# Kernel tuning notes

Hardware: AMD Instinct MI355X
Metric: run time of the kernel (lower is better)

## Reference

```python
import jax, jax.numpy as jnp
import numpy as np
import math

B, N, M, Lx = 8, 32, 16, 32
D, TE_DIM, IN_DIM, TT = 64, 16, 17, 63   # hid_dim, te_dim, 1+te_dim, hid_dim-1
H, DH, NL = 4, 16, 2
TAU, DELTA = 60.0, 300.0                 # tau, 5 minutes in seconds
P = B * N * M


def _ln(x, g, b):
    mu = x.mean(-1, keepdims=True)
    v = ((x - mu) ** 2).mean(-1, keepdims=True)
    return (x - mu) / jnp.sqrt(v + 1e-5) * g + b


def _time_bias():
    idx = jnp.arange(M)
    dist = jnp.abs(idx[:, None] - idx[None, :]).astype(jnp.float32) * DELTA
    return jnp.log(jnp.exp(-dist / TAU) + 1e-12)


def _pos_enc():
    pos = jnp.arange(M, dtype=jnp.float32)[:, None]
    div = jnp.exp(jnp.arange(0, D, 2, dtype=jnp.float32) * (-math.log(10000.0) / D))
    pe = jnp.zeros((M, D))
    pe = pe.at[:, 0::2].set(jnp.sin(pos * div))
    pe = pe.at[:, 1::2].set(jnp.cos(pos * div))
    return pe


def _heads(t):   # (b, m, D) -> (b, H, m, DH)
    b, m, _ = t.shape
    return t.reshape(b, m, H, DH).transpose(0, 2, 1, 3)


def _merge(t):   # (b, H, m, DH) -> (b, m, D)
    b, _, m, _ = t.shape
    return t.transpose(0, 2, 1, 3).reshape(b, m, D)


def _patch_gattn(x, pm, qw, qb, kw, kb, vw, vb, ow, ob, tbias):
    q, k, v = _heads(x @ qw.T + qb), _heads(x @ kw.T + kb), _heads(x @ vw.T + vb)
    a = jnp.einsum('bhqd,bhkd->bhqk', q, k) / math.sqrt(DH) + tbias[None, None]
    a = jnp.where((pm == 0.0)[:, None, None, :], -1e9, a)
    out = _merge(jnp.einsum('bhqk,bhkd->bhqd', jax.nn.softmax(a, -1), v))
    return (out @ ow.T + ob) * pm[..., None]


def _mha(q_in, kv_in, in_w, in_b, ow, ob, kpm=None):
    wq, wk, wv = in_w[:D], in_w[D:2 * D], in_w[2 * D:]
    bq, bk, bv = in_b[:D], in_b[D:2 * D], in_b[2 * D:]
    q = _heads(q_in @ wq.T + bq)
    k = _heads(kv_in @ wk.T + bk)
    v = _heads(kv_in @ wv.T + bv)
    a = jnp.einsum('bhqd,bhkd->bhqk', q, k) / math.sqrt(DH)
    if kpm is not None:
        a = jnp.where(kpm[:, None, None, :], -1e9, a)
    out = _merge(jnp.einsum('bhqk,bhkd->bhqd', jax.nn.softmax(a, -1), v))
    return out @ ow.T + ob


def _forward(x, mask, ttcn_w1, ttcn_b1, ttcn_w2, ttcn_b2, ttcn_w3, ttcn_b3, t_bias,
             ga_qw, ga_qb, ga_kw, ga_kb, ga_vw, ga_vb, ga_ow, ga_ob,
             tf_in_w, tf_in_b, tf_out_w, tf_out_b, tf_ln1_g, tf_ln1_b, tf_ln2_g, tf_ln2_b,
             tf_fw1, tf_fb1, tf_fw2, tf_fb2,
             q_embed, cls_in_w, cls_in_b, cls_out_w, cls_out_b, logit_w, logit_b):
    m = mask.astype(x.dtype)                          # (P, Lx, 1)
    # --- TTCN: per-sample dynamic filter generation + masked seq-softmax agg ---
    h = jax.nn.relu(x @ ttcn_w1.T + ttcn_b1)
    h = jax.nn.relu(h @ ttcn_w2.T + ttcn_b2)
    filt = h @ ttcn_w3.T + ttcn_b3                    # (P, Lx, IN_DIM*TT)
    filt = filt * m + (1.0 - m) * (-1e8)
    fs = jax.nn.softmax(filt, axis=1).reshape(P, Lx, TT, IN_DIM)
    h_t = jax.nn.relu(jnp.einsum('pli,plti->pt', x, fs) + t_bias)   # (P, TT)
    mask_patch = (m.sum(axis=1) > 0).astype(x.dtype)  # (P, 1)
    xp = jnp.concatenate([h_t, mask_patch], -1).reshape(B, N, M, D)
    pm = mask_patch.reshape(B, N, M)
    tbias = _time_bias()
    pe = _pos_enc()
    xc = xp
    for l in range(NL):
        if l > 0:
            x_last = xc
        xb = xc.reshape(B * N, M, D)
        pmb = pm.reshape(B * N, M)
        xb = xb + _patch_gattn(xb, pmb, ga_qw[l], ga_qb[l], ga_kw[l], ga_kb[l],
                               ga_vw[l], ga_vb[l], ga_ow[l], ga_ob[l], tbias)
        xb = xb + pe[None]
        # post-norm TransformerEncoderLayer (tf_layer = 1, no attn mask, eval mode)
        attn = _mha(xb, xb, tf_in_w[l], tf_in_b[l], tf_out_w[l], tf_out_b[l])
        xb = _ln(xb + attn, tf_ln1_g[l], tf_ln1_b[l])
        ff = jax.nn.relu(xb @ tf_fw1[l].T + tf_fb1[l]) @ tf_fw2[l].T + tf_fb2[l]
        xb = _ln(xb + ff, tf_ln2_g[l], tf_ln2_b[l])
        xc = xb.reshape(B, N, M, D)
        if l > 0:
            xc = x_last + xc
    x_seq = xc.mean(axis=1)                            # (B, M, D)
    kpm = ~((pm > 0).any(axis=1))                      # (B, M), True = padded
    qs = jnp.broadcast_to(q_embed[None], (B, 5, D))
    z = _mha(qs, x_seq, cls_in_w, cls_in_b, cls_out_w, cls_out_b, kpm=kpm)
    return (z @ logit_w.T + logit_b)[..., 0]           # (B, 5)


def setup_inputs() -> dict:
    key = jax.random.key(0)
    ks = iter(jax.random.split(key, 64))
    def rn(shape, s=0.1):
        return jax.random.normal(next(ks), shape, jnp.float32) * s
    inp = {
        'x': jax.random.normal(next(ks), (P, Lx, IN_DIM), jnp.float32),
        'mask': jax.random.randint(next(ks), (P, Lx, 1), 0, 2, jnp.int32),
        'ttcn_w1': rn((TT, IN_DIM)), 'ttcn_b1': jnp.zeros((TT,)),
        'ttcn_w2': rn((TT, TT)), 'ttcn_b2': jnp.zeros((TT,)),
        'ttcn_w3': rn((IN_DIM * TT, TT)), 'ttcn_b3': jnp.zeros((IN_DIM * TT,)),
        't_bias': rn((1, TT)),
        'ga_qw': rn((NL, D, D)), 'ga_qb': jnp.zeros((NL, D)),
        'ga_kw': rn((NL, D, D)), 'ga_kb': jnp.zeros((NL, D)),
        'ga_vw': rn((NL, D, D)), 'ga_vb': jnp.zeros((NL, D)),
        'ga_ow': rn((NL, D, D)), 'ga_ob': jnp.zeros((NL, D)),
        'tf_in_w': rn((NL, 3 * D, D)), 'tf_in_b': jnp.zeros((NL, 3 * D)),
        'tf_out_w': rn((NL, D, D)), 'tf_out_b': jnp.zeros((NL, D)),
        'tf_ln1_g': jnp.ones((NL, D)), 'tf_ln1_b': jnp.zeros((NL, D)),
        'tf_ln2_g': jnp.ones((NL, D)), 'tf_ln2_b': jnp.zeros((NL, D)),
        'tf_fw1': rn((NL, 2048, D)), 'tf_fb1': jnp.zeros((NL, 2048)),
        'tf_fw2': rn((NL, D, 2048)), 'tf_fb2': jnp.zeros((NL, D)),
        'q_embed': rn((5, D), 1.0),
        'cls_in_w': rn((3 * D, D)), 'cls_in_b': jnp.zeros((3 * D,)),
        'cls_out_w': rn((D, D)), 'cls_out_b': jnp.zeros((D,)),
        'logit_w': rn((1, D)), 'logit_b': jnp.zeros((1,)),
    }
    return inp


def reference(x, mask, ttcn_w1, ttcn_b1, ttcn_w2, ttcn_b2, ttcn_w3, ttcn_b3, t_bias,
              ga_qw, ga_qb, ga_kw, ga_kb, ga_vw, ga_vb, ga_ow, ga_ob,
              tf_in_w, tf_in_b, tf_out_w, tf_out_b, tf_ln1_g, tf_ln1_b, tf_ln2_g, tf_ln2_b,
              tf_fw1, tf_fb1, tf_fw2, tf_fb2,
              q_embed, cls_in_w, cls_in_b, cls_out_w, cls_out_b, logit_w, logit_b):
    return _forward(x, mask, ttcn_w1, ttcn_b1, ttcn_w2, ttcn_b2, ttcn_w3, ttcn_b3, t_bias,
                    ga_qw, ga_qb, ga_kw, ga_kb, ga_vw, ga_vb, ga_ow, ga_ob,
                    tf_in_w, tf_in_b, tf_out_w, tf_out_b, tf_ln1_g, tf_ln1_b, tf_ln2_g, tf_ln2_b,
                    tf_fw1, tf_fb1, tf_fw2, tf_fb2,
                    q_embed, cls_in_w, cls_in_b, cls_out_w, cls_out_b, logit_w, logit_b)
```

## Files before the change

kernel.cpp:

```cpp
#include <hip/hip_runtime.h>
#include <hip/hip_bf16.h>
#include <math.h>

#define B_  8
#define N_  32
#define M_  16
#define LX  32
#define D_  64
#define IN_DIM_ 17
#define TT_ 63
#define H_  4
#define DH_ 16
#define P_TOT 4096
#define BN_ 256
#define FF_ 2048

#define FRAG_TOT 83200
#define OFF_INW  2048
#define OFF_OUTW 3584
#define OFF_FW1  4096
#define OFF_FW2  20480

typedef unsigned short ushort_t;
typedef __attribute__((ext_vector_type(8))) short short8;
typedef __attribute__((ext_vector_type(4))) float floatx4;

#define MFMA16(a,b,c) __builtin_amdgcn_mfma_f32_16x16x32_bf16((a),(b),(c),0,0,0)

__device__ __forceinline__ float fast_exp2(float x){
#if __has_builtin(__builtin_amdgcn_exp2f)
  return __builtin_amdgcn_exp2f(x);
#else
  return __expf(x * 0.6931471805599453f);
#endif
}
__device__ __forceinline__ float fast_rcp(float x){
#if __has_builtin(__builtin_amdgcn_rcpf)
  return __builtin_amdgcn_rcpf(x);
#else
  return 1.0f / x;
#endif
}

__device__ __forceinline__ ushort_t f2bf(float f){
  unsigned u = __float_as_uint(f);
  u += 0x7FFFu + ((u >> 16) & 1u);
  return (ushort_t)(u >> 16);
}
__device__ __forceinline__ float bf2f(ushort_t h){ return __uint_as_float(((unsigned)h) << 16); }

__device__ __forceinline__ uint4 pack8(const ushort_t* h){
  uint4 u;
  u.x = (unsigned)h[0] | ((unsigned)h[1] << 16);
  u.y = (unsigned)h[2] | ((unsigned)h[3] << 16);
  u.z = (unsigned)h[4] | ((unsigned)h[5] << 16);
  u.w = (unsigned)h[6] | ((unsigned)h[7] << 16);
  return u;
}

__device__ __forceinline__ void split8(const float* r, short8& hi, short8& lo){
  #pragma unroll
  for (int j = 0; j < 8; ++j){
    float v = r[j];
    ushort_t h = f2bf(v);
    ushort_t l2 = f2bf(v - bf2f(h));
    hi[j] = (short)h; lo[j] = (short)l2;
  }
}
__device__ __forceinline__ uint4 cvt8(const float* r){
  ushort_t hh[8];
  #pragma unroll
  for (int j = 0; j < 8; ++j) hh[j] = f2bf(r[j]);
  return pack8(hh);
}
__device__ __forceinline__ short8 cvt8s(const float* r){
  union { uint4 u4; short8 s8; } cv;
  cv.u4 = cvt8(r);
  return cv.s8;
}

__device__ __forceinline__ floatx4 mm3(short8 ah, short8 al, short8 bh, short8 bl, floatx4 c){
  c = MFMA16(ah, bh, c); c = MFMA16(ah, bl, c); c = MFMA16(al, bh, c); return c;
}

__device__ __forceinline__ float dot64(const float* __restrict__ a, const float* __restrict__ w){
  const float4* a4 = (const float4*)a;
  const float4* w4 = (const float4*)w;
  float acc = 0.f;
  #pragma unroll
  for (int k = 0; k < 16; ++k){ float4 x = a4[k], y = w4[k];
    acc += x.x*y.x + x.y*y.y + x.z*y.z + x.w*y.w; }
  return acc;
}
__device__ __forceinline__ float dot16(const float* __restrict__ a, const float* __restrict__ b){
  const float4* a4 = (const float4*)a; const float4* b4 = (const float4*)b;
  float acc = 0.f;
  #pragma unroll
  for (int k = 0; k < 4; ++k){ float4 x = a4[k], y = b4[k];
    acc += x.x*y.x + x.y*y.y + x.z*y.z + x.w*y.w; }
  return acc;
}

__device__ __forceinline__ void packA68(const float* buf, short8* fA, int tid){
  if (tid < 128){
    int ln = tid & 63, ks = tid >> 6;
    const float* r = buf + (ln & 15)*68 + ks*32 + ((ln >> 4) & 3)*8;
    short8 hi, lo; split8(r, hi, lo);
    fA[tid] = hi; fA[128 + tid] = lo;
  }
}

__global__ __launch_bounds__(256) void prep_kernel(
    const float* __restrict__ w1, const float* __restrict__ w2, const float* __restrict__ w3,
    const float* __restrict__ gqw, const float* __restrict__ gkw,
    const float* __restrict__ gvw, const float* __restrict__ gow,
    const float* __restrict__ inw, const float* __restrict__ outw,
    const float* __restrict__ fw1, const float* __restrict__ fw2,
    uint4* __restrict__ fr)
{
  int s = blockIdx.x*256 + threadIdx.x;
  if (s >= FRAG_TOT) return;
  const float* src; int Nr, Kr, KS, rel; int w3seg = 0, noLo = 0;
  if (s < 256)      { src = w1; Nr=63;  Kr=17; KS=1; rel = s; noLo = 1; }
  else if (s < 768) { src = w2; Nr=63;  Kr=63; KS=2; rel = s-256; noLo = 1; }
  else if (s < 9472){ src = w3; Nr=1071;Kr=63; KS=2; rel = s-768; w3seg = 1; noLo = 1; }
  else {
    int t = s - 9472, l = t / 36864, r2 = t - l*36864;
    if (r2 < 512)        { src = gqw + l*4096;   Nr=64;  Kr=64;   KS=2;  rel = r2; }
    else if (r2 < 1024)  { src = gkw + l*4096;   Nr=64;  Kr=64;   KS=2;  rel = r2-512; }
    else if (r2 < 1536)  { src = gvw + l*4096;   Nr=64;  Kr=64;   KS=2;  rel = r2-1024; }
    else if (r2 < 2048)  { src = gow + l*4096;   Nr=64;  Kr=64;   KS=2;  rel = r2-1536; }
    else if (r2 < 3584)  { src = inw + l*12288;  Nr=192; Kr=64;   KS=2;  rel = r2-2048; }
    else if (r2 < 4096)  { src = outw + l*4096;  Nr=64;  Kr=64;   KS=2;  rel = r2-3584; }
    else if (r2 < 20480) { src = fw1 + l*131072; Nr=2048;Kr=64;   KS=2;  rel = r2-4096; noLo = 1; }
    else                 { src = fw2 + l*131072; Nr=64;  Kr=2048; KS=64; rel = r2-20480; noLo = 1; }
  }
  int lane = rel & 63, tmp = rel >> 6;
  int ks = tmp % KS, nt = tmp / KS;
  int kb = ks*32 + ((lane >> 4) & 3)*8;
  int n, validn;
  if (w3seg){
    int i = nt >> 2, tq = nt & 3;
    int t = tq*16 + (lane & 15);
    n = t*17 + i;
    validn = (t < 63);
  } else {
    n = nt*16 + (lane & 15);
    validn = (n < Nr);
  }
  float v[8];
  #pragma unroll
  for (int j = 0; j < 8; ++j){
    v[j] = (validn && (kb + j) < Kr) ? src[n*Kr + kb + j] : 0.f;
    if (w3seg){
      if ((kb + j) == 63) v[j] = 1.0f;
      v[j] *= 1.4426950408889634f;
    }
  }
  ushort_t hh[8];
  #pragma unroll
  for (int j = 0; j < 8; ++j) hh[j] = f2bf(v[j]);
  fr[s] = pack8(hh);
  if (!noLo){
    ushort_t ll[8];
    #pragma unroll
    for (int j = 0; j < 8; ++j) ll[j] = f2bf(v[j] - bf2f(hh[j]));
    fr[FRAG_TOT + s] = pack8(ll);
  }
}

__global__ __launch_bounds__(256) void ttcn_kernel(
    const float* __restrict__ x, const int* __restrict__ mask,
    const float* __restrict__ b1, const float* __restrict__ b2,
    const float* __restrict__ tb,
    const short8* __restrict__ w1bhi,
    const short8* __restrict__ w2bhi,
    const short8* __restrict__ w3bhi,
    float* __restrict__ xp, float* __restrict__ pm)
{
  __shared__ __align__(16) char pool[16512];
  float*    xs    = (float*)(pool + 0);
  float*    xst   = (float*)(pool + 2560);
  float*    msv   = (float*)(pool + 5008);
  float*    xsumv = (float*)(pool + 5136);
  short8*   xfhi  = (short8*)(pool + 5216);
  ushort_t* h1t   = (ushort_t*)(pool + 7264);
  ushort_t* h2t   = (ushort_t*)(pool + 11872);

  const int p = blockIdx.x, tid = threadIdx.x;
  const int lane = tid & 63, wvi = tid >> 6;
  const int nidx = lane & 15, quad = lane >> 4;

  for (int idx = tid; idx < LX*IN_DIM_; idx += 256){
    int l = (idx * 3856) >> 16;
    int i = idx - l*17;
    xs[l*20 + i] = x[p*(LX*IN_DIM_) + idx];
  }
  if (tid < LX) msv[tid] = (float)mask[p*LX + tid];
  __syncthreads();

  if (tid < 128){
    int mt = tid >> 6;
    int l = mt*16 + nidx;
    float r[8];
    #pragma unroll
    for (int j = 0; j < 8; ++j){
      int k = quad*8 + j;
      r[j] = (k < IN_DIM_) ? xs[l*20 + k] : 0.f;
    }
    ((uint4*)xfhi)[tid] = cvt8(r);
  } else {
    if (tid < 128 + IN_DIM_){
      int i = tid - 128;
      float s = 0.f;
      #pragma unroll
      for (int l = 0; l < LX; ++l) s += xs[l*20 + i];
      xsumv[i] = s;
    }
    for (int idx = tid - 128; idx < 544; idx += 128){
      int i = idx >> 5, l = idx & 31;
      xst[i*36 + l] = xs[l*20 + i];
    }
  }
  __syncthreads();

  {
    short8 axh0 = xfhi[lane], axh1 = xfhi[64 + lane];
    short8 bh = w1bhi[wvi*64 + lane];
    floatx4 a0 = {0.f,0.f,0.f,0.f}, a1 = {0.f,0.f,0.f,0.f};
    a0 = MFMA16(axh0, bh, a0);
    a1 = MFMA16(axh1, bh, a1);
    int t = wvi*16 + nidx;
    float bb = (t < TT_) ? b1[t] : 0.f;
    #pragma unroll
    for (int r = 0; r < 4; ++r){
      h1t[(quad*4+r)*72 + t]      = f2bf(fmaxf(a0[r] + bb, 0.f));
      h1t[(16+quad*4+r)*72 + t]   = f2bf(fmaxf(a1[r] + bb, 0.f));
    }
  }
  __syncthreads();

  {
    short8 ah[2][2];
    #pragma unroll
    for (int mt = 0; mt < 2; ++mt)
      #pragma unroll
      for (int ks = 0; ks < 2; ++ks){
        int l = mt*16 + nidx;
        ah[mt][ks] = *(const short8*)((const char*)h1t + (l*72 + ks*32 + quad*8)*2);
      }
    short8 bh0 = w2bhi[(wvi*2+0)*64 + lane];
    short8 bh1 = w2bhi[(wvi*2+1)*64 + lane];
    floatx4 a0 = {0.f,0.f,0.f,0.f}, a1 = {0.f,0.f,0.f,0.f};
    a0 = MFMA16(ah[0][0], bh0, a0); a0 = MFMA16(ah[0][1], bh1, a0);
    a1 = MFMA16(ah[1][0], bh0, a1); a1 = MFMA16(ah[1][1], bh1, a1);
    int t = wvi*16 + nidx;
    float bb = (t < TT_) ? b2[t] : 0.f;
    #pragma unroll
    for (int r = 0; r < 4; ++r){
      h2t[(quad*4+r)*72 + t]      = f2bf(fmaxf(a0[r] + bb, 0.f));
      h2t[(16+quad*4+r)*72 + t]   = f2bf(fmaxf(a1[r] + bb, 0.f));
    }
  }
  __syncthreads();

  {
    short8 ah[2][2];
    #pragma unroll
    for (int mt = 0; mt < 2; ++mt)
      #pragma unroll
      for (int ks = 0; ks < 2; ++ks){
        int l = mt*16 + nidx;
        ah[mt][ks] = *(const short8*)((const char*)h2t + (l*72 + ks*32 + quad*8)*2);
      }
    if (quad == 3){
      ah[0][1][7] = (short)((msv[nidx]      == 0.f) ? f2bf(-1e8f) : (ushort_t)0);
      ah[1][1][7] = (short)((msv[16 + nidx] == 0.f) ? f2bf(-1e8f) : (ushort_t)0);
    }
    const int t_out = wvi*16 + nidx;
    const int rA = quad*4;
    float acc_t = 0.f;
    short8 nbh0 = w3bhi[(wvi*2+0)*64 + lane];
    short8 nbh1 = w3bhi[(wvi*2+1)*64 + lane];
    for (int it = 0; it < 17; ++it){
      short8 bh0 = nbh0, bh1 = nbh1;
      if (it < 16){
        int nt = wvi + it*4 + 4;
        nbh0 = w3bhi[(nt*2+0)*64 + lane];
        nbh1 = w3bhi[(nt*2+1)*64 + lane];
      }
      floatx4 a0 = {0.f,0.f,0.f,0.f}, a1 = {0.f,0.f,0.f,0.f};
      a0 = MFMA16(ah[0][0], bh0, a0); a0 = MFMA16(ah[0][1], bh1, a0);
      a1 = MFMA16(ah[1][0], bh0, a1); a1 = MFMA16(ah[1][1], bh1, a1);

      const float4 xA = *(const float4*)(xst + it*36 + rA);
      const float4 xB = *(const float4*)(xst + it*36 + rA + 16);
      float den0 = 0.f, den1 = 0.f, num0 = 0.f, num1 = 0.f;
      float e;
      e = fast_exp2(a0[0]); den0 += e; num0 = fmaf(e, xA.x, num0);
      e = fast_exp2(a0[1]); den0 += e; num0 = fmaf(e, xA.y, num0);
      e = fast_exp2(a0[2]); den0 += e; num0 = fmaf(e, xA.z, num0);
      e = fast_exp2(a0[3]); den0 += e; num0 = fmaf(e, xA.w, num0);
      e = fast_exp2(a1[0]); den1 += e; num1 = fmaf(e, xB.x, num1);
      e = fast_exp2(a1[1]); den1 += e; num1 = fmaf(e, xB.y, num1);
      e = fast_exp2(a1[2]); den1 += e; num1 = fmaf(e, xB.z, num1);
      e = fast_exp2(a1[3]); den1 += e; num1 = fmaf(e, xB.w, num1);
      float den = den0 + den1, num = num0 + num1;
      den += __shfl_xor(den, 16, 64); den += __shfl_xor(den, 32, 64);
      num += __shfl_xor(num, 16, 64); num += __shfl_xor(num, 32, 64);
      float res = (den > 0.f) ? num * fast_rcp(den) : xsumv[it] * (1.f/32.f);
      acc_t += res;
    }
    if (quad == 0 && t_out < TT_)
      xp[p*D_ + t_out] = fmaxf(acc_t + tb[t_out], 0.f);
  }
  if (tid == 63){
    float s = 0.f;
    #pragma unroll
    for (int l = 0; l < LX; ++l) s += msv[l];
    float mp = (s > 0.f) ? 1.f : 0.f;
    xp[p*D_ + TT_] = mp;
    pm[p] = mp;
  }
}

__global__ __launch_bounds__(256) void layer12_kernel(
    const float* __restrict__ xin, const float* __restrict__ pm,
    const short8* __restrict__ frS,
    const float* __restrict__ gqb, const float* __restrict__ gkb,
    const float* __restrict__ gvb, const float* __restrict__ gob,
    const float* __restrict__ inb, const float* __restrict__ outb,
    const float* __restrict__ ln1g, const float* __restrict__ ln1b,
    const float* __restrict__ fb1, const float* __restrict__ fb2,
    const float* __restrict__ ln2g, const float* __restrict__ ln2b,
    float* __restrict__ xout)
{
  __shared__ __align__(16) float xb[16*68];
  __shared__ __align__(16) float xb2[16*68];
  __shared__ __align__(16) float q_[16*68];
  __shared__ __align__(16) float k_[16*68];
  __shared__ __align__(16) float v_[16*68];
  __shared__ __align__(16) float ao[16*68];
  __shared__ __align__(16) float ss[1024];
  __shared__ __align__(16) short8 fragA[256];
  __shared__ __align__(16) float hbuf[4*16*36];
  __shared__ __align__(16) float part[4*16*68];
  __shared__ __align__(16) float pe_t[1024];
  __shared__ float tbt[16];
  __shared__ float pmv[16], mur[16], rvr[16];

  const int bn = blockIdx.x, tid = threadIdx.x;
  const int lane = tid & 63, wvi = tid >> 6;
  const int nidx = lane & 15, quad = lane >> 4;
  const float* xin_p = xin + bn*1024;

  for (int o = tid; o < 1024; o += 256) xb[(o>>6)*68 + (o&63)] = xin_p[o];
  if (tid < 16) pmv[tid] = pm[bn*16 + tid];
  for (int o = tid; o < 1024; o += 256){
    int tok = o >> 6, d = o & 63;
    float div = __expf((float)(d & ~1) * (-0.14391156831212793f));
    float arg = (float)tok * div;
    pe_t[o] = (d & 1) ? cosf(arg) : sinf(arg);
  }
  if (tid >= 32 && tid < 48) tbt[tid-32] = logf(expf(-5.0f*(float)(tid-32)) + 1e-12f);
  __syncthreads();

  for (int l = 0; l < 2; ++l){
    const int lbase = 9472 + l*36864;
    const float* gqbL = gqb + l*64;  const float* gkbL = gkb + l*64;
    const float* gvbL = gvb + l*64;  const float* gobL = gob + l*64;
    const float* inbL = inb + l*192; const float* outbL = outb + l*64;
    const float* ln1gL = ln1g + l*64; const float* ln1bL = ln1b + l*64;
    const float* fb1L = fb1 + l*2048; const float* fb2L = fb2 + l*64;
    const float* ln2gL = ln2g + l*64; const float* ln2bL = ln2b + l*64;

    float xres[4];
    #pragma unroll
    for (int kk2 = 0; kk2 < 4; ++kk2){
      int o = tid + kk2*256;
      xres[kk2] = xb[(o>>6)*68 + (o&63)];
    }

    short8 gb[3][4], ob4[4], mb[3][4];
    #pragma unroll
    for (int mat = 0; mat < 3; ++mat){
      int base = lbase + mat*512;
      gb[mat][0] = frS[base + (wvi*2+0)*64 + lane];
      gb[mat][1] = frS[FRAG_TOT + base + (wvi*2+0)*64 + lane];
      gb[mat][2] = frS[base + (wvi*2+1)*64 + lane];
      gb[mat][3] = frS[FRAG_TOT + base + (wvi*2+1)*64 + lane];
    }
    {
      int base = lbase + 1536;
      ob4[0] = frS[base + (wvi*2+0)*64 + lane];
      ob4[1] = frS[FRAG_TOT + base + (wvi*2+0)*64 + lane];
      ob4[2] = frS[base + (wvi*2+1)*64 + lane];
      ob4[3] = frS[FRAG_TOT + base + (wvi*2+1)*64 + lane];
    }
    #pragma unroll
    for (int sel = 0; sel < 3; ++sel){
      int base = lbase + OFF_INW + (sel*4 + wvi)*128;
      mb[sel][0] = frS[base + lane];
      mb[sel][1] = frS[FRAG_TOT + base + lane];
      mb[sel][2] = frS[base + 64 + lane];
      mb[sel][3] = frS[FRAG_TOT + base + 64 + lane];
    }

    packA68(xb, fragA, tid);
    __syncthreads();
    {
      short8 axh0 = fragA[lane], axh1 = fragA[64+lane];
      short8 axl0 = fragA[128+lane], axl1 = fragA[192+lane];
      #pragma unroll
      for (int mat = 0; mat < 3; ++mat){
        floatx4 c = {0.f,0.f,0.f,0.f};
        c = mm3(axh0, axl0, gb[mat][0], gb[mat][1], c);
        c = mm3(axh1, axl1, gb[mat][2], gb[mat][3], c);
        int d = wvi*16 + nidx;
        float bb = (mat == 0 ? gqbL : mat == 1 ? gkbL : gvbL)[d];
        float* dst = (mat == 0 ? q_ : mat == 1 ? k_ : v_);
        #pragma unroll
        for (int r = 0; r < 4; ++r) dst[(quad*4+r)*68 + d] = c[r] + bb;
      }
    }
    __syncthreads();
    {
      int row = tid >> 2;
      int h = row >> 4, qm = row & 15;
      int km0 = (tid & 3) * 4;
      float s4[4];
      #pragma unroll
      for (int j = 0; j < 4; ++j){
        int km = km0 + j;
        float acc = dot16(q_ + qm*68 + h*16, k_ + km*68 + h*16);
        int dd = qm - km; if (dd < 0) dd = -dd;
        acc = acc * 0.25f + tbt[dd];
        if (pmv[km] == 0.f) acc = -1e9f;
        s4[j] = acc;
      }
      float mx = fmaxf(fmaxf(s4[0], s4[1]), fmaxf(s4[2], s4[3]));
      mx = fmaxf(mx, __shfl_xor(mx, 1, 64));
      mx = fmaxf(mx, __shfl_xor(mx, 2, 64));
      float e4[4], se = 0.f;
      #pragma unroll
      for (int j = 0; j < 4; ++j){ e4[j] = __expf(s4[j]-mx); se += e4[j]; }
      se += __shfl_xor(se, 1, 64);
      se += __shfl_xor(se, 2, 64);
      float inv = fast_rcp(se);
      #pragma unroll
      for (int j = 0; j < 4; ++j) ss[row*16 + km0 + j] = e4[j]*inv;
    }
    __syncthreads();
    for (int o = tid; o < 1024; o += 256){
      int m = o >> 6, d = o & 63, h = d >> 4;
      float acc = 0.f;
      #pragma unroll
      for (int km = 0; km < 16; ++km) acc += ss[h*256 + m*16 + km] * v_[km*68 + d];
      ao[m*68 + d] = acc;
    }
    __syncthreads();
    packA68(ao, fragA, tid);
    __syncthreads();
    {
      short8 axh0 = fragA[lane], axh1 = fragA[64+lane];
      short8 axl0 = fragA[128+lane], axl1 = fragA[192+lane];
      floatx4 c = {0.f,0.f,0.f,0.f};
      c = mm3(axh0, axl0, ob4[0], ob4[1], c);
      c = mm3(axh1, axl1, ob4[2], ob4[3], c);
      int d = wvi*16 + nidx;
      float bb = gobL[d];
      #pragma unroll
      for (int r = 0; r < 4; ++r){
        int tok = quad*4 + r;
        xb[tok*68 + d] += (c[r] + bb) * pmv[tok] + pe_t[tok*64 + d];
      }
    }
    __syncthreads();

    short8 mob[4], f1c[4], f2c[4];
    {
      int base = lbase + OFF_OUTW;
      mob[0] = frS[base + (wvi*2+0)*64 + lane];
      mob[1] = frS[FRAG_TOT + base + (wvi*2+0)*64 + lane];
      mob[2] = frS[base + (wvi*2+1)*64 + lane];
      mob[3] = frS[FRAG_TOT + base + (wvi*2+1)*64 + lane];
    }
    {
      int f1base = lbase + OFF_FW1, f2base = lbase + OFF_FW2;
      #pragma unroll
      for (int t2 = 0; t2 < 2; ++t2){
        int sb = f1base + ((wvi*32+t2)*2)*64 + lane;
        f1c[t2*2+0] = frS[sb];
        f1c[t2*2+1] = frS[sb + 64];
      }
      #pragma unroll
      for (int ntd = 0; ntd < 4; ++ntd)
        f2c[ntd] = frS[f2base + (ntd*64 + wvi*16)*64 + lane];
    }

    packA68(xb, fragA, tid);
    __syncthreads();
    {
      short8 axh0 = fragA[lane], axh1 = fragA[64+lane];
      short8 axl0 = fragA[128+lane], axl1 = fragA[192+lane];
      #pragma unroll
      for (int sel = 0; sel < 3; ++sel){
        floatx4 c = {0.f,0.f,0.f,0.f};
        c = mm3(axh0, axl0, mb[sel][0], mb[sel][1], c);
        c = mm3(axh1, axl1, mb[sel][2], mb[sel][3], c);
        int d = wvi*16 + nidx;
        float bb = inbL[(sel*4 + wvi)*16 + nidx];
        float* dst = (sel == 0 ? q_ : sel == 1 ? k_ : v_);
        #pragma unroll
        for (int r = 0; r < 4; ++r) dst[(quad*4+r)*68 + d] = c[r] + bb;
      }
    }
    __syncthreads();
    {
      int row = tid >> 2;
      int h = row >> 4, qm = row & 15;
      int km0 = (tid & 3) * 4;
      float s4[4];
      #pragma unroll
      for (int j = 0; j < 4; ++j)
        s4[j] = 0.25f * dot16(q_ + qm*68 + h*16, k_ + (km0+j)*68 + h*16);
      float mx = fmaxf(fmaxf(s4[0], s4[1]), fmaxf(s4[2], s4[3]));
      mx = fmaxf(mx, __shfl_xor(mx, 1, 64));
      mx = fmaxf(mx, __shfl_xor(mx, 2, 64));
      float e4[4], se = 0.f;
      #pragma unroll
      for (int j = 0; j < 4; ++j){ e4[j] = __expf(s4[j]-mx); se += e4[j]; }
      se += __shfl_xor(se, 1, 64);
      se += __shfl_xor(se, 2, 64);
      float inv = fast_rcp(se);
      #pragma unroll
      for (int j = 0; j < 4; ++j) ss[row*16 + km0 + j] = e4[j]*inv;
    }
    __syncthreads();
    for (int o = tid; o < 1024; o += 256){
      int m = o >> 6, d = o & 63, h = d >> 4;
      float acc = 0.f;
      #pragma unroll
      for (int km = 0; km < 16; ++km) acc += ss[h*256 + m*16 + km] * v_[km*68 + d];
      ao[m*68 + d] = acc;
    }
    __syncthreads();
    packA68(ao, fragA, tid);
    __syncthreads();
    {
      short8 axh0 = fragA[lane], axh1 = fragA[64+lane];
      short8 axl0 = fragA[128+lane], axl1 = fragA[192+lane];
      floatx4 c = {0.f,0.f,0.f,0.f};
      c = mm3(axh0, axl0, mob[0], mob[1], c);
      c = mm3(axh1, axl1, mob[2], mob[3], c);
      int d = wvi*16 + nidx;
      float bb = outbL[d];
      #pragma unroll
      for (int r = 0; r < 4; ++r) xb[(quad*4+r)*68 + d] += c[r] + bb;
    }
    __syncthreads();

    if (tid < 64){
      int row = tid >> 2, seg = tid & 3;
      const float* rp = xb + row*68 + seg*16;
      float s = 0.f;
      #pragma unroll
      for (int j = 0; j < 16; ++j) s += rp[j];
      s += __shfl_xor(s, 1, 64); s += __shfl_xor(s, 2, 64);
      float mu = s * (1.f/64.f);
      float v = 0.f;
      #pragma unroll
      for (int j = 0; j < 16; ++j){ float t = rp[j]-mu; v += t*t; }
      v += __shfl_xor(v, 1, 64); v += __shfl_xor(v, 2, 64);
      if (seg == 0){ mur[row] = mu; rvr[row] = rsqrtf(v*(1.f/64.f) + 1e-5f); }
    }
    __syncthreads();
    for (int o = tid; o < 1024; o += 256){
      int m = o >> 6, d = o & 63;
      xb2[m*68 + d] = (xb[m*68 + d] - mur[m]) * rvr[m] * ln1gL[d] + ln1bL[d];
    }
    __syncthreads();
    packA68(xb2, fragA, tid);
    __syncthreads();

    {
      const int w = wvi;
      const int f1base = lbase + OFF_FW1, f2base = lbase + OFF_FW2;
      short8 axh0 = fragA[lane], axh1 = fragA[64 + lane];
      floatx4 y0 = {0.f,0.f,0.f,0.f}, y1 = y0, y2 = y0, y3 = y0;
      float* hw = hbuf + w*576;

      short8 f1n[4], f2n[4];
      for (int it = 0; it < 16; ++it){
        int ntA = w*32 + it*2;
        floatx4 hA = {0.f,0.f,0.f,0.f}, hB = hA;
        hA = MFMA16(axh0, f1c[0], hA); hA = MFMA16(axh1, f1c[1], hA);
        hB = MFMA16(axh0, f1c[2], hB); hB = MFMA16(axh1, f1c[3], hB);
        float bbA = fb1L[ntA*16 + nidx], bbB = fb1L[ntA*16 + 16 + nidx];
        #pragma unroll
        for (int r = 0; r < 4; ++r){
          hw[(quad*4+r)*36 + nidx]      = fmaxf(hA[r] + bbA, 0.f);
          hw[(quad*4+r)*36 + 16 + nidx] = fmaxf(hB[r] + bbB, 0.f);
        }
        if (it < 15){
          int ntN = ntA + 2, kstN = w*16 + it + 1;
          #pragma unroll
          for (int t2 = 0; t2 < 2; ++t2){
            int sb = f1base + ((ntN+t2)*2)*64 + lane;
            f1n[t2*2+0] = frS[sb];
            f1n[t2*2+1] = frS[sb + 64];
          }
          #pragma unroll
          for (int ntd = 0; ntd < 4; ++ntd)
            f2n[ntd] = frS[f2base + (ntd*64 + kstN)*64 + lane];
        }
        short8 ah = cvt8s(hw + (lane & 15)*36 + quad*8);
        y0 = MFMA16(ah, f2c[0], y0);
        y1 = MFMA16(ah, f2c[1], y1);
        y2 = MFMA16(ah, f2c[2], y2);
        y3 = MFMA16(ah, f2c[3], y3);
        #pragma unroll
        for (int j = 0; j < 4; ++j){ f1c[j] = f1n[j]; f2c[j] = f2n[j]; }
      }
      #pragma unroll
      for (int r = 0; r < 4; ++r){
        int row = (quad*4 + r)*68;
        part[w*1088 + row + nidx]      = y0[r];
        part[w*1088 + row + 16 + nidx] = y1[r];
        part[w*1088 + row + 32 + nidx] = y2[r];
        part[w*1088 + row + 48 + nidx] = y3[r];
      }
    }
    __syncthreads();
    for (int o = tid; o < 1024; o += 256){
      int tok = o >> 6, d = o & 63;
      float s = xb2[tok*68 + d] + fb2L[d];
      #pragma unroll
      for (int ww = 0; ww < 4; ++ww) s += part[ww*1088 + tok*68 + d];
      xb[tok*68 + d] = s;
    }
    __syncthreads();
    if (tid < 64){
      int row = tid >> 2, seg = tid & 3;
      const float* rp = xb + row*68 + seg*16;
      float s = 0.f;
      #pragma unroll
      for (int j = 0; j < 16; ++j) s += rp[j];
      s += __shfl_xor(s, 1, 64); s += __shfl_xor(s, 2, 64);
      float mu = s * (1.f/64.f);
      float v = 0.f;
      #pragma unroll
      for (int j = 0; j < 16; ++j){ float t = rp[j]-mu; v += t*t; }
      v += __shfl_xor(v, 1, 64); v += __shfl_xor(v, 2, 64);
      if (seg == 0){ mur[row] = mu; rvr[row] = rsqrtf(v*(1.f/64.f) + 1e-5f); }
    }
    __syncthreads();
    #pragma unroll
    for (int kk2 = 0; kk2 < 4; ++kk2){
      int o = tid + kk2*256;
      int tok = o >> 6, d = o & 63;
      float vv = (xb[tok*68 + d] - mur[tok]) * rvr[tok] * ln2gL[d] + ln2bL[d];
      if (l == 0) xb[tok*68 + d] = vv;
      else        xout[bn*1024 + o] = vv + xres[kk2];
    }
    __syncthreads();
  }
}

__global__ __launch_bounds__(256) void final_kernel(
    const float* __restrict__ xc, const float* __restrict__ pm,
    const float* __restrict__ q_embed,
    const float* __restrict__ cin_w, const float* __restrict__ cin_b,
    const float* __restrict__ cout_w, const float* __restrict__ cout_b,
    const float* __restrict__ logit_w, const float* __restrict__ logit_b,
    float* __restrict__ out)
{
  const int b = blockIdx.x;
  const int tid = threadIdx.x;
  __shared__ __align__(16) float xs[M_ * D_];
  __shared__ float kpmv[M_];
  __shared__ __align__(16) float qv[5 * D_], kv[M_ * D_], vv[M_ * D_];
  __shared__ float sv[H_ * 5 * M_];
  __shared__ __align__(16) float ao[5 * D_], zv[5 * D_];

  for (int o = tid; o < M_ * D_; o += 256) {
    int m = o >> 6, d = o & 63;
    float acc = 0.f;
    #pragma unroll
    for (int n = 0; n < N_; ++n) acc += xc[(((b * N_ + n) * M_ + m) * D_) + d];
    xs[o] = acc * (1.f / 32.f);
  }
  if (tid < M_) {
    float any = 0.f;
    #pragma unroll
    for (int n = 0; n < N_; ++n) any += (pm[(b * N_ + n) * M_ + tid] > 0.f) ? 1.f : 0.f;
    kpmv[tid] = (any > 0.f) ? 0.f : 1.f;
  }
  __syncthreads();

  for (int o = tid; o < 5 * D_; o += 256) {
    int qi = o >> 6, d = o & 63;
    qv[o] = cin_b[d] + dot64(q_embed + qi * D_, cin_w + d * D_);
  }
  for (int o = tid; o < 2 * M_ * D_; o += 256) {
    int sel = o >> 10, r = o & 1023, m = r >> 6, d = r & 63;
    float acc = cin_b[D_ + sel * D_ + d] + dot64(xs + m * D_, cin_w + (D_ + sel * D_ + d) * D_);
    ((sel == 0) ? kv : vv)[r] = acc;
  }
  __syncthreads();

  for (int o = tid; o < H_ * 5 * M_; o += 256) {
    int h = o / 80, r = o % 80, qi = r >> 4, km = r & 15;
    float acc = 0.25f * dot16(qv + qi * D_ + h * DH_, kv + km * D_ + h * DH_);
    if (kpmv[km] != 0.f) acc = -1e9f;
    sv[o] = acc;
  }
  __syncthreads();
  if (tid < H_ * 5) {
    int h = tid / 5, qi = tid % 5;
    float* row = sv + h * 80 + qi * M_;
    float mx = -1e30f;
    #pragma unroll
    for (int km = 0; km < M_; ++km) mx = fmaxf(mx, row[km]);
    float se = 0.f;
    #pragma unroll
    for (int km = 0; km < M_; ++km) { float e = __expf(row[km] - mx); row[km] = e; se += e; }
    float inv = 1.f / se;
    #pragma unroll
    for (int km = 0; km < M_; ++km) row[km] *= inv;
  }
  __syncthreads();
  for (int o = tid; o < 5 * D_; o += 256) {
    int qi = o >> 6, d = o & 63, h = d >> 4;
    float acc = 0.f;
    #pragma unroll
    for (int km = 0; km < M_; ++km) acc += sv[h * 80 + qi * M_ + km] * vv[km * D_ + d];
    ao[o] = acc;
  }
  __syncthreads();
  for (int o = tid; o < 5 * D_; o += 256) {
    int qi = o >> 6, d = o & 63;
    zv[o] = cout_b[d] + dot64(ao + qi * D_, cout_w + d * D_);
  }
  __syncthreads();
  if (tid < 5) {
    float acc = logit_b[0] + dot64(zv + tid * D_, logit_w);
    out[b * 5 + tid] = acc;
  }
}

extern "C" void kernel_launch(void* const* d_in, const int* in_sizes, int n_in,
                              void* d_out, int out_size, void* d_ws, size_t ws_size,
                              hipStream_t stream) {
  const float* x       = (const float*)d_in[0];
  const int*   mask    = (const int*)  d_in[1];
  const float* ttcn_w1 = (const float*)d_in[2];
  const float* ttcn_b1 = (const float*)d_in[3];
  const float* ttcn_w2 = (const float*)d_in[4];
  const float* ttcn_b2 = (const float*)d_in[5];
  const float* ttcn_w3 = (const float*)d_in[6];
  const float* ttcn_b3 = (const float*)d_in[7];
  const float* t_bias  = (const float*)d_in[8];
  const float* ga_qw   = (const float*)d_in[9];
  const float* ga_qb   = (const float*)d_in[10];
  const float* ga_kw   = (const float*)d_in[11];
  const float* ga_kb   = (const float*)d_in[12];
  const float* ga_vw   = (const float*)d_in[13];
  const float* ga_vb   = (const float*)d_in[14];
  const float* ga_ow   = (const float*)d_in[15];
  const float* ga_ob   = (const float*)d_in[16];
  const float* tf_in_w = (const float*)d_in[17];
  const float* tf_in_b = (const float*)d_in[18];
  const float* tf_out_w= (const float*)d_in[19];
  const float* tf_out_b= (const float*)d_in[20];
  const float* tf_ln1g = (const float*)d_in[21];
  const float* tf_ln1b = (const float*)d_in[22];
  const float* tf_ln2g = (const float*)d_in[23];
  const float* tf_ln2b = (const float*)d_in[24];
  const float* tf_fw1  = (const float*)d_in[25];
  const float* tf_fb1  = (const float*)d_in[26];
  const float* tf_fw2  = (const float*)d_in[27];
  const float* tf_fb2  = (const float*)d_in[28];
  const float* q_embed = (const float*)d_in[29];
  const float* cls_in_w  = (const float*)d_in[30];
  const float* cls_in_b  = (const float*)d_in[31];
  const float* cls_out_w = (const float*)d_in[32];
  const float* cls_out_b = (const float*)d_in[33];
  const float* logit_w = (const float*)d_in[34];
  const float* logit_b = (const float*)d_in[35];
  (void)ttcn_b3;

  float* wsf  = (float*)d_ws;
  float* xp   = wsf;
  float* pmb  = wsf + P_TOT * D_;
  float* xbuf = pmb + P_TOT;
  uint4* fr   = (uint4*)(xbuf + P_TOT * D_);
  const short8* frS = (const short8*)fr;

  prep_kernel<<<325, 256, 0, stream>>>(ttcn_w1, ttcn_w2, ttcn_w3,
      ga_qw, ga_kw, ga_vw, ga_ow, tf_in_w, tf_out_w, tf_fw1, tf_fw2, fr);

  ttcn_kernel<<<P_TOT, 256, 0, stream>>>(x, mask, ttcn_b1, ttcn_b2, t_bias,
      frS + 0, frS + 256, frS + 768,
      xp, pmb);

  layer12_kernel<<<BN_, 256, 0, stream>>>(xp, pmb, frS,
      ga_qb, ga_kb, ga_vb, ga_ob, tf_in_b, tf_out_b, tf_ln1g, tf_ln1b,
      tf_fb1, tf_fb2, tf_ln2g, tf_ln2b, xbuf);

  final_kernel<<<B_, 256, 0, stream>>>(xbuf, pmb, q_embed,
                                       cls_in_w, cls_in_b, cls_out_w, cls_out_b,
                                       logit_w, logit_b, (float*)d_out);
}
```

Measured before the change: 235.2 us.

## Compact valid timesteps in TTCN and skip second M-tile when at most 16 valid

The TTCN kernel builds a ballot-based compaction map of unmasked timesteps and gathers only valid rows into the MFMA input tiles. When 16 or fewer timesteps are valid, it runs a single 16-row tile through all three matmuls and the softmax reduction, halving MFMA and exp work for that block. Padding rows beyond the valid count are masked via the bias slot instead of reading the mask array. This adds branching and a gather indirection, and relies on the mask density of inputs for benefit.

```diff
diff --git a/kernel.cpp b/kernel.cpp
--- a/kernel.cpp
+++ b/kernel.cpp
@@ -181,8 +181,9 @@
   __shared__ __align__(16) char pool[16512];
   float*    xs    = (float*)(pool + 0);
   float*    xst   = (float*)(pool + 2560);
-  float*    msv   = (float*)(pool + 5008);
+  int*      cmap  = (int*)  (pool + 5008);
   float*    xsumv = (float*)(pool + 5136);
+  int*      Vp    = (int*)  (pool + 5204);
   short8*   xfhi  = (short8*)(pool + 5216);
   ushort_t* h1t   = (ushort_t*)(pool + 7264);
   ushort_t* h2t   = (ushort_t*)(pool + 11872);
@@ -196,19 +197,30 @@
     int i = idx - l*17;
     xs[l*20 + i] = x[p*(LX*IN_DIM_) + idx];
   }
-  if (tid < LX) msv[tid] = (float)mask[p*LX + tid];
-  __syncthreads();
+  if (tid < 64){
+    int mv = (tid < 32) ? mask[p*LX + tid] : 0;
+    unsigned long long bal = __ballot(mv != 0);
+    if (tid < 32) cmap[tid] = 0;
+    int pos = __popcll(bal & ((1ull << tid) - 1ull));
+    if (mv != 0) cmap[pos] = tid;
+    if (tid == 0) *Vp = (int)__popcll(bal);
+  }
+  __syncthreads();
+  const int V   = *Vp;
+  const int two = (V > 16);
 
   if (tid < 128){
     int mt = tid >> 6;
-    int l = mt*16 + nidx;
-    float r[8];
-    #pragma unroll
-    for (int j = 0; j < 8; ++j){
-      int k = quad*8 + j;
-      r[j] = (k < IN_DIM_) ? xs[l*20 + k] : 0.f;
-    }
-    ((uint4*)xfhi)[tid] = cvt8(r);
+    if (mt == 0 || two){
+      int lc = cmap[mt*16 + nidx];
+      float r[8];
+      #pragma unroll
+      for (int j = 0; j < 8; ++j){
+        int k = quad*8 + j;
+        r[j] = (k < IN_DIM_) ? xs[lc*20 + k] : 0.f;
+      }
+      ((uint4*)xfhi)[tid] = cvt8(r);
+    }
   } else {
     if (tid < 128 + IN_DIM_){
       int i = tid - 128;
@@ -217,108 +229,142 @@
       for (int l = 0; l < LX; ++l) s += xs[l*20 + i];
       xsumv[i] = s;
     }
-    for (int idx = tid - 128; idx < 544; idx += 128){
-      int i = idx >> 5, l = idx & 31;
-      xst[i*36 + l] = xs[l*20 + i];
+    if (two){
+      for (int idx = tid - 128; idx < 544; idx += 128){
+        int i = idx >> 5, cl = idx & 31;
+        xst[i*36 + cl] = xs[cmap[cl]*20 + i];
+      }
+    } else {
+      for (int idx = tid - 128; idx < 272; idx += 128){
+        int i = idx >> 4, cl = idx & 15;
+        xst[i*36 + cl] = xs[cmap[cl]*20 + i];
+      }
     }
   }
   __syncthreads();
 
   {
-    short8 axh0 = xfhi[lane], axh1 = xfhi[64 + lane];
+    short8 axh0 = xfhi[lane];
     short8 bh = w1bhi[wvi*64 + lane];
-    floatx4 a0 = {0.f,0.f,0.f,0.f}, a1 = {0.f,0.f,0.f,0.f};
+    floatx4 a0 = {0.f,0.f,0.f,0.f};
     a0 = MFMA16(axh0, bh, a0);
-    a1 = MFMA16(axh1, bh, a1);
     int t = wvi*16 + nidx;
     float bb = (t < TT_) ? b1[t] : 0.f;
-    #pragma unroll
-    for (int r = 0; r < 4; ++r){
-      h1t[(quad*4+r)*72 + t]      = f2bf(fmaxf(a0[r] + bb, 0.f));
-      h1t[(16+quad*4+r)*72 + t]   = f2bf(fmaxf(a1[r] + bb, 0.f));
-    }
+    if (two){
+      short8 axh1 = xfhi[64 + lane];
+      floatx4 a1 = {0.f,0.f,0.f,0.f};
+      a1 = MFMA16(axh1, bh, a1);
+      #pragma unroll
+      for (int r = 0; r < 4; ++r)
+        h1t[(16+quad*4+r)*72 + t] = f2bf(fmaxf(a1[r] + bb, 0.f));
+    }
+    #pragma unroll
+    for (int r = 0; r < 4; ++r)
+      h1t[(quad*4+r)*72 + t] = f2bf(fmaxf(a0[r] + bb, 0.f));
   }
   __syncthreads();
 
   {
-    short8 ah[2][2];
-    #pragma unroll
-    for (int mt = 0; mt < 2; ++mt)
-      #pragma unroll
-      for (int ks = 0; ks < 2; ++ks){
-        int l = mt*16 + nidx;
-        ah[mt][ks] = *(const short8*)((const char*)h1t + (l*72 + ks*32 + quad*8)*2);
-      }
     short8 bh0 = w2bhi[(wvi*2+0)*64 + lane];
     short8 bh1 = w2bhi[(wvi*2+1)*64 + lane];
-    floatx4 a0 = {0.f,0.f,0.f,0.f}, a1 = {0.f,0.f,0.f,0.f};
-    a0 = MFMA16(ah[0][0], bh0, a0); a0 = MFMA16(ah[0][1], bh1, a0);
-    a1 = MFMA16(ah[1][0], bh0, a1); a1 = MFMA16(ah[1][1], bh1, a1);
+    short8 a00 = *(const short8*)((const char*)h1t + (nidx*72 + quad*8)*2);
+    short8 a01 = *(const short8*)((const char*)h1t + (nidx*72 + 32 + quad*8)*2);
+    floatx4 a0 = {0.f,0.f,0.f,0.f};
+    a0 = MFMA16(a00, bh0, a0); a0 = MFMA16(a01, bh1, a0);
     int t = wvi*16 + nidx;
     float bb = (t < TT_) ? b2[t] : 0.f;
-    #pragma unroll
-    for (int r = 0; r < 4; ++r){
-      h2t[(quad*4+r)*72 + t]      = f2bf(fmaxf(a0[r] + bb, 0.f));
-      h2t[(16+quad*4+r)*72 + t]   = f2bf(fmaxf(a1[r] + bb, 0.f));
-    }
+    if (two){
+      short8 a10 = *(const short8*)((const char*)h1t + ((16+nidx)*72 + quad*8)*2);
+      short8 a11 = *(const short8*)((const char*)h1t + ((16+nidx)*72 + 32 + quad*8)*2);
+      floatx4 a1 = {0.f,0.f,0.f,0.f};
+      a1 = MFMA16(a10, bh0, a1); a1 = MFMA16(a11, bh1, a1);
+      #pragma unroll
+      for (int r = 0; r < 4; ++r)
+        h2t[(16+quad*4+r)*72 + t] = f2bf(fmaxf(a1[r] + bb, 0.f));
+    }
+    #pragma unroll
+    for (int r = 0; r < 4; ++r)
+      h2t[(quad*4+r)*72 + t] = f2bf(fmaxf(a0[r] + bb, 0.f));
   }
   __syncthreads();
 
   {
-    short8 ah[2][2];
-    #pragma unroll
-    for (int mt = 0; mt < 2; ++mt)
-      #pragma unroll
-      for (int ks = 0; ks < 2; ++ks){
-        int l = mt*16 + nidx;
-        ah[mt][ks] = *(const short8*)((const char*)h2t + (l*72 + ks*32 + quad*8)*2);
-      }
+    short8 ah0[2], ah1[2];
+    #pragma unroll
+    for (int ks = 0; ks < 2; ++ks)
+      ah0[ks] = *(const short8*)((const char*)h2t + (nidx*72 + ks*32 + quad*8)*2);
+    if (two){
+      #pragma unroll
+      for (int ks = 0; ks < 2; ++ks)
+        ah1[ks] = *(const short8*)((const char*)h2t + ((16+nidx)*72 + ks*32 + quad*8)*2);
+    }
     if (quad == 3){
-      ah[0][1][7] = (short)((msv[nidx]      == 0.f) ? f2bf(-1e8f) : (ushort_t)0);
-      ah[1][1][7] = (short)((msv[16 + nidx] == 0.f) ? f2bf(-1e8f) : (ushort_t)0);
+      if (two) ah1[1][7] = (short)((16 + nidx >= V) ? f2bf(-1e8f) : (ushort_t)0);
+      else     ah0[1][7] = (short)((nidx >= V)      ? f2bf(-1e8f) : (ushort_t)0);
     }
     const int t_out = wvi*16 + nidx;
     const int rA = quad*4;
     float acc_t = 0.f;
     short8 nbh0 = w3bhi[(wvi*2+0)*64 + lane];
     short8 nbh1 = w3bhi[(wvi*2+1)*64 + lane];
-    for (int it = 0; it < 17; ++it){
-      short8 bh0 = nbh0, bh1 = nbh1;
-      if (it < 16){
-        int nt = wvi + it*4 + 4;
-        nbh0 = w3bhi[(nt*2+0)*64 + lane];
-        nbh1 = w3bhi[(nt*2+1)*64 + lane];
-      }
-      floatx4 a0 = {0.f,0.f,0.f,0.f}, a1 = {0.f,0.f,0.f,0.f};
-      a0 = MFMA16(ah[0][0], bh0, a0); a0 = MFMA16(ah[0][1], bh1, a0);
-      a1 = MFMA16(ah[1][0], bh0, a1); a1 = MFMA16(ah[1][1], bh1, a1);
-
-      const float4 xA = *(const float4*)(xst + it*36 + rA);
-      const float4 xB = *(const float4*)(xst + it*36 + rA + 16);
-      float den0 = 0.f, den1 = 0.f, num0 = 0.f, num1 = 0.f;
-      float e;
-      e = fast_exp2(a0[0]); den0 += e; num0 = fmaf(e, xA.x, num0);
-      e = fast_exp2(a0[1]); den0 += e; num0 = fmaf(e, xA.y, num0);
-      e = fast_exp2(a0[2]); den0 += e; num0 = fmaf(e, xA.z, num0);
-      e = fast_exp2(a0[3]); den0 += e; num0 = fmaf(e, xA.w, num0);
-      e = fast_exp2(a1[0]); den1 += e; num1 = fmaf(e, xB.x, num1);
-      e = fast_exp2(a1[1]); den1 += e; num1 = fmaf(e, xB.y, num1);
-      e = fast_exp2(a1[2]); den1 += e; num1 = fmaf(e, xB.z, num1);
-      e = fast_exp2(a1[3]); den1 += e; num1 = fmaf(e, xB.w, num1);
-      float den = den0 + den1, num = num0 + num1;
-      den += __shfl_xor(den, 16, 64); den += __shfl_xor(den, 32, 64);
-      num += __shfl_xor(num, 16, 64); num += __shfl_xor(num, 32, 64);
-      float res = (den > 0.f) ? num * fast_rcp(den) : xsumv[it] * (1.f/32.f);
-      acc_t += res;
+    if (two){
+      for (int it = 0; it < 17; ++it){
+        short8 bh0 = nbh0, bh1 = nbh1;
+        if (it < 16){
+          int nt = wvi + it*4 + 4;
+          nbh0 = w3bhi[(nt*2+0)*64 + lane];
+          nbh1 = w3bhi[(nt*2+1)*64 + lane];
+        }
+        floatx4 a0 = {0.f,0.f,0.f,0.f}, a1 = {0.f,0.f,0.f,0.f};
+        a0 = MFMA16(ah0[0], bh0, a0); a0 = MFMA16(ah0[1], bh1, a0);
+        a1 = MFMA16(ah1[0], bh0, a1); a1 = MFMA16(ah1[1], bh1, a1);
+
+        const float4 xA = *(const float4*)(xst + it*36 + rA);
+        const float4 xB = *(const float4*)(xst + it*36 + rA + 16);
+        float den0 = 0.f, den1 = 0.f, num0 = 0.f, num1 = 0.f;
+        float e;
+        e = fast_exp2(a0[0]); den0 += e; num0 = fmaf(e, xA.x, num0);
+        e = fast_exp2(a0[1]); den0 += e; num0 = fmaf(e, xA.y, num0);
+        e = fast_exp2(a0[2]); den0 += e; num0 = fmaf(e, xA.z, num0);
+        e = fast_exp2(a0[3]); den0 += e; num0 = fmaf(e, xA.w, num0);
+        e = fast_exp2(a1[0]); den1 += e; num1 = fmaf(e, xB.x, num1);
+        e = fast_exp2(a1[1]); den1 += e; num1 = fmaf(e, xB.y, num1);
+        e = fast_exp2(a1[2]); den1 += e; num1 = fmaf(e, xB.z, num1);
+        e = fast_exp2(a1[3]); den1 += e; num1 = fmaf(e, xB.w, num1);
+        float den = den0 + den1, num = num0 + num1;
+        den += __shfl_xor(den, 16, 64); den += __shfl_xor(den, 32, 64);
+        num += __shfl_xor(num, 16, 64); num += __shfl_xor(num, 32, 64);
+        float res = (den > 0.f) ? num * fast_rcp(den) : xsumv[it] * (1.f/32.f);
+        acc_t += res;
+      }
+    } else {
+      for (int it = 0; it < 17; ++it){
+        short8 bh0 = nbh0, bh1 = nbh1;
+        if (it < 16){
+          int nt = wvi + it*4 + 4;
+          nbh0 = w3bhi[(nt*2+0)*64 + lane];
+          nbh1 = w3bhi[(nt*2+1)*64 + lane];
+        }
+        floatx4 a0 = {0.f,0.f,0.f,0.f};
+        a0 = MFMA16(ah0[0], bh0, a0); a0 = MFMA16(ah0[1], bh1, a0);
+
+        const float4 xA = *(const float4*)(xst + it*36 + rA);
+        float den = 0.f, num = 0.f, e;
+        e = fast_exp2(a0[0]); den += e; num = fmaf(e, xA.x, num);
+        e = fast_exp2(a0[1]); den += e; num = fmaf(e, xA.y, num);
+        e = fast_exp2(a0[2]); den += e; num = fmaf(e, xA.z, num);
+        e = fast_exp2(a0[3]); den += e; num = fmaf(e, xA.w, num);
+        den += __shfl_xor(den, 16, 64); den += __shfl_xor(den, 32, 64);
+        num += __shfl_xor(num, 16, 64); num += __shfl_xor(num, 32, 64);
+        float res = (den > 0.f) ? num * fast_rcp(den) : xsumv[it] * (1.f/32.f);
+        acc_t += res;
+      }
     }
     if (quad == 0 && t_out < TT_)
       xp[p*D_ + t_out] = fmaxf(acc_t + tb[t_out], 0.f);
   }
-  if (tid == 63){
-    float s = 0.f;
-    #pragma unroll
-    for (int l = 0; l < LX; ++l) s += msv[l];
-    float mp = (s > 0.f) ? 1.f : 0.f;
+  if (tid == 0){
+    float mp = (V > 0) ? 1.f : 0.f;
     xp[p*D_ + TT_] = mp;
     pm[p] = mp;
   }
```

New measurement: 233.2 us. No clear change (-0.8%).
